# Kernel optimization log

Measured on AMD Instinct MI355X. Metric: run time of the kernel, lower is better.

## Reference

```python
import jax, jax.numpy as jnp
import numpy as np

B, T, P = 256, 1024, 32
HOME = 0  # home_idx from init_kwargs


def setup_inputs() -> dict:
    key = jax.random.key(0)
    k1, k2 = jax.random.split(key, 2)
    U = jax.random.normal(k1, (B, T, P), dtype=jnp.float32)
    A = jax.random.uniform(k2, (P, P), dtype=jnp.float32, minval=-0.01, maxval=0.01)
    bias = jnp.zeros((P,), dtype=jnp.float32)
    return {"unary_logits_btp": U, "A": A, "bias": bias}


def reference(unary_logits_btp, A, bias):
    """Constrained Viterbi decode (enforce at least one non-home state).
    State is (purpose p, visited-nonhome flag v in {0,1}). Returns paths (B,T) int32."""
    U = unary_logits_btp + bias  # (B,T,P), bias broadcast as in decode()
    Bn, Tn, Pn = U.shape
    NEG = jnp.finfo(U.dtype).min / 4
    is_home = jnp.arange(Pn) == HOME  # (P,)

    # t=0: v=0 only at home, v=1 only at non-home
    d0 = jnp.where(is_home, U[:, 0], NEG)
    d1 = jnp.where(is_home, NEG, U[:, 0])
    delta0 = jnp.stack([d0, d1], axis=-1)  # (B,P,2)

    def step(delta, U_t):
        # prev{v}[b, q, p] = delta[b, q, v] + A[q, p]
        prev0 = delta[:, :, 0][:, :, None] + A  # (B,P,P)
        prev1 = delta[:, :, 1][:, :, None] + A
        a0 = jnp.argmax(prev0, axis=1).astype(jnp.int32)
        v0 = jnp.max(prev0, axis=1)  # (B,P)
        a1 = jnp.argmax(prev1, axis=1).astype(jnp.int32)
        v1 = jnp.max(prev1, axis=1)
        use1 = v1 > v0  # strict >, matching torch.where(val_from1 > val_from0, ...)
        bval = jnp.where(use1, v1, v0)
        bq = jnp.where(use1, a1, a0)
        bv = use1.astype(jnp.int32)
        # next v=0 reachable only at home (from prev v=0)
        dn0 = jnp.where(is_home, v0 + U_t, NEG)
        # next v=1: home from prev v=1; non-home from best of prev v=0/v=1
        dn1 = jnp.where(is_home, v1, bval) + U_t
        p1 = jnp.where(is_home, a1, bq)
        vv1 = jnp.where(is_home, 1, bv).astype(jnp.int32)
        delta_new = jnp.stack([dn0, dn1], axis=-1)          # (B,P,2)
        psi_p = jnp.stack([a0, p1], axis=-1)                # (B,P,2) best prev purpose
        psi_v = jnp.stack([jnp.zeros_like(vv1), vv1], -1)   # (B,P,2) best prev flag
        return delta_new, (psi_p, psi_v)

    Us = jnp.swapaxes(U, 0, 1)  # (T,B,P)
    delta_T, (psi_p, psi_v) = jax.lax.scan(step, delta0, Us[1:])  # psi_*: (T-1,B,P,2)

    last_p = jnp.argmax(delta_T[:, :, 1], axis=1).astype(jnp.int32)  # (B,)
    b_idx = jnp.arange(Bn)

    def back(carry, psi):
        y, v = carry  # (B,), (B,)
        pp, pv = psi  # (B,P,2)
        py = pp[b_idx, y, v]
        nv = pv[b_idx, y, v]
        return (py, nv), py

    _, ys = jax.lax.scan(back, (last_p, jnp.ones((Bn,), jnp.int32)), (psi_p, psi_v),
                         reverse=True)  # ys: (T-1,B) with ys[t] = y[t]
    paths = jnp.concatenate([jnp.swapaxes(ys, 0, 1), last_p[:, None]], axis=1)  # (B,T)
    return paths
```

## Files before the change

### kernel.cpp

```cpp
#include <hip/hip_runtime.h>

#define T_LEN 1024
#define P_DIM 32
#define HOME_IDX 0
#define NCHUNK 32
#define CHUNK 32


__launch_bounds__(1024, 1)
__global__ void crf_viterbi_kernel(const float* __restrict__ U,
                                   const float* __restrict__ A,
                                   const float* __restrict__ bias,
                                   int* __restrict__ out)
{
    __shared__ __align__(16) float sdelta[P_DIM];
    __shared__ unsigned char spsi[(T_LEN - 1) * P_DIM];
    __shared__ unsigned char Mmap[NCHUNK * P_DIM];
    __shared__ unsigned char ent[NCHUNK];
    __shared__ int last_p_sh;

    const int tid = threadIdx.x;
    const int b   = blockIdx.x;
    int* __restrict__ outb = out + (size_t)b * T_LEN;

    if (tid < 64) {
        const int lane = tid;
        const int p    = lane & 31;
        const int h    = lane >> 5;
        const float NEG = -(3.4028234663852886e38f / 4.0f);

        float Areg[16];
#pragma unroll
        for (int j = 0; j < 16; ++j)
            Areg[j] = A[(16 * h + j) * P_DIM + p];
        const float A0p    = A[p];
        const float A00    = A[0];
        const float bias_p = bias[p];
        const float bias0  = bias[0];
        const int   q0     = h << 4;
        const bool  is_home = (p == HOME_IDX);

        const float4* __restrict__ sd4 = (const float4*)sdelta;

        const float* __restrict__ Ub = U + (size_t)b * T_LEN * P_DIM;

        const float u00 = Ub[p] + bias_p;
        float delta1  = is_home ? NEG : u00;
        float delta0h = Ub[HOME_IDX] + bias0;

        float L0 = Ub[1 * P_DIM + p];
        float L1 = Ub[2 * P_DIM + p];
        float L2 = Ub[3 * P_DIM + p];
        float L3 = Ub[4 * P_DIM + p];

        float Ut_n = L0 + bias_p;
        float u0_n = __shfl(Ut_n, 0);

        sdelta[p] = delta1;
        float4 R0 = sd4[4 * h + 0];
        float4 R1 = sd4[4 * h + 1];
        float4 R2 = sd4[4 * h + 2];
        float4 R3 = sd4[4 * h + 3];

#define STEP(t, Lc, Lr) do {                                                   \
    const float Ut  = Ut_n;                                                    \
    const float u0c = u0_n;                                                    \
    Ut_n = (Lc) + bias_p;                                                      \
    u0_n = __shfl(Ut_n, 0);                                                    \
    { int tn = (t) + 4; if (tn > T_LEN - 1) tn = T_LEN - 1;                    \
      (Lr) = Ub[(size_t)tn * P_DIM + p]; }                                     \
    float c[16];                                                               \
    c[0]  = R0.x + Areg[0];  c[1]  = R0.y + Areg[1];                           \
    c[2]  = R0.z + Areg[2];  c[3]  = R0.w + Areg[3];                           \
    c[4]  = R1.x + Areg[4];  c[5]  = R1.y + Areg[5];                           \
    c[6]  = R1.z + Areg[6];  c[7]  = R1.w + Areg[7];                           \
    c[8]  = R2.x + Areg[8];  c[9]  = R2.y + Areg[9];                           \
    c[10] = R2.z + Areg[10]; c[11] = R2.w + Areg[11];                          \
    c[12] = R3.x + Areg[12]; c[13] = R3.y + Areg[13];                          \
    c[14] = R3.z + Areg[14]; c[15] = R3.w + Areg[15];                          \
       \
    const float g0 = fmaxf(fmaxf(c[0],  c[1]),  c[2]);                         \
    const float g1 = fmaxf(fmaxf(c[3],  c[4]),  c[5]);                         \
    const float g2 = fmaxf(fmaxf(c[6],  c[7]),  c[8]);                         \
    const float g3 = fmaxf(fmaxf(c[9],  c[10]), c[11]);                        \
    const float g4 = fmaxf(fmaxf(c[12], c[13]), c[14]);                        \
    const float h0 = fmaxf(fmaxf(g0, g1), g2);                                 \
    const float h1 = fmaxf(fmaxf(g3, g4), c[15]);                              \
    const float bv = fmaxf(h0, h1);                                            \
                                                 \
    const float ovv = __shfl_xor(bv, 32);                                      \
    const float v1  = fmaxf(bv, ovv);                                          \
    const float v0  = delta0h + A0p;                                           \
    const bool  use1 = (v1 > v0);                    \
    const bool  cond = use1 || is_home;                                        \
    const float sel  = cond ? v1 : v0;                                         \
    const float dn1  = sel + Ut;                                               \
    delta0h = (delta0h + A00) + u0c;                                           \
       \
        \
    sdelta[p] = dn1;                                                           \
    R0 = sd4[4 * h + 0];                                                       \
    R1 = sd4[4 * h + 1];                                                       \
    R2 = sd4[4 * h + 2];                                                       \
    R3 = sd4[4 * h + 3];                                                       \
           \
    int ia = 99;                                                               \
    _Pragma("unroll")                                                          \
    for (int j = 15; j >= 0; --j)                                              \
        if (c[j] == v1) ia = q0 + j;                                           \
    const int oia = __shfl_xor(ia, 32);                                        \
    const int a1  = (ia < oia) ? ia : oia;                                     \
    const int bt  = cond ? (a1 | 32) : 0;                                      \
    spsi[(size_t)((t) - 1) * P_DIM + p] = (unsigned char)bt;                   \
    delta1 = dn1;                                                              \
} while (0)

        STEP(1, L1, L0);
        STEP(2, L2, L1);
        STEP(3, L3, L2);
        for (int t = 4; t <= T_LEN - 4; t += 4) {
            STEP(t + 0, L0, L3);
            STEP(t + 1, L1, L0);
            STEP(t + 2, L2, L1);
            STEP(t + 3, L3, L2);
        }
#undef STEP

        float mv = delta1;
        int   mi = p;
#pragma unroll
        for (int m = 16; m >= 1; m >>= 1) {
            float ov = __shfl_xor(mv, m);
            int   oi = __shfl_xor(mi, m);
            bool take = (ov > mv) || ((ov == mv) && (oi < mi));
            mv = take ? ov : mv;
            mi = take ? oi : mi;
        }
        if (lane == 0) {
            outb[T_LEN - 1] = mi;
            last_p_sh = mi;
        }
    }

    __syncthreads();

    {
        const int c  = tid >> 5;
        const int pp = tid & 31;
        const int i_hi = min((c + 1) * CHUNK, T_LEN - 1);
        const int i_lo = c * CHUNK;
        int y = pp, v = 1;
        for (int i = i_hi - 1; i >= i_lo; --i) {
            const int bt = spsi[i * P_DIM + y];
            const int py = v ? (bt & 31) : 0;
            const int nv = v ? ((bt >> 5) & 1) : 0;
            y = py; v = nv;
        }
        Mmap[c * P_DIM + pp] = (unsigned char)(y | (v << 5));
    }
    __syncthreads();

    if (tid == 0) {
        int y = last_p_sh, v = 1;
        for (int c = NCHUNK - 1; c >= 0; --c) {
            ent[c] = (unsigned char)(y | (v << 5));
            if (v) {
                const int m = Mmap[c * P_DIM + y];
                y = m & 31;
                v = (m >> 5) & 1;
            } else {
                y = 0; v = 0;
            }
        }
    }
    __syncthreads();

    if (tid < NCHUNK) {
        const int c = tid;
        const int i_hi = min((c + 1) * CHUNK, T_LEN - 1);
        const int i_lo = c * CHUNK;
        const int e = ent[c];
        int y = e & 31;
        int v = (e >> 5) & 1;
        for (int i = i_hi - 1; i >= i_lo; --i) {
            const int bt = spsi[i * P_DIM + y];
            const int py = v ? (bt & 31) : 0;
            const int nv = v ? ((bt >> 5) & 1) : 0;
            outb[i] = py;
            y = py; v = nv;
        }
    }
}

extern "C" void kernel_launch(void* const* d_in, const int* in_sizes, int n_in,
                              void* d_out, int out_size, void* d_ws, size_t ws_size,
                              hipStream_t stream) {
    const float* U    = (const float*)d_in[0];
    const float* A    = (const float*)d_in[1];
    const float* bias = (const float*)d_in[2];
    int* out = (int*)d_out;

    const int B = in_sizes[0] / (T_LEN * P_DIM);
    crf_viterbi_kernel<<<B, 1024, 0, stream>>>(U, A, bias, out);
}
```

Baseline: 309.2 us.

## Software-pipeline argmax backpointer computation across Viterbi steps

Defers the per-step argmax index search and backpointer store to the following steps, using double-buffered candidate arrays so the index search for step t overlaps the max chain of step t+1. The argmax now compares against each half's local max (not the combined max) and picks the winning half, which takes the index search off the critical serial dependency. It adds register pressure from two 16-float candidate arrays plus carried state, and epilogue code to drain the pipeline.

```diff
diff --git a/kernel.cpp b/kernel.cpp
--- a/kernel.cpp
+++ b/kernel.cpp
@@ -41,7 +41,6 @@
         const bool  is_home = (p == HOME_IDX);
 
         const float4* __restrict__ sd4 = (const float4*)sdelta;
-
         const float* __restrict__ Ub = U + (size_t)b * T_LEN * P_DIM;
 
         const float u00 = Ub[p] + bias_p;
@@ -62,69 +61,102 @@
         float4 R2 = sd4[4 * h + 2];
         float4 R3 = sd4[4 * h + 3];
 
-#define STEP(t, Lc, Lr) do {                                                   \
+        float cA[16], cB[16];
+        float bvp = 0.f, ovvp = 0.f, bv2 = 0.f, ovv2 = 0.f;
+        bool  condp = false, cond2 = false;
+        int   ia2 = 0, io2 = 0;
+
+#define STEP(t, F1, F2, CC, CP, Lc, Lr) do {                                   \
     const float Ut  = Ut_n;                                                    \
     const float u0c = u0_n;                                                    \
-    Ut_n = (Lc) + bias_p;                                                      \
-    u0_n = __shfl(Ut_n, 0);                                                    \
-    { int tn = (t) + 4; if (tn > T_LEN - 1) tn = T_LEN - 1;                    \
-      (Lr) = Ub[(size_t)tn * P_DIM + p]; }                                     \
-    float c[16];                                                               \
-    c[0]  = R0.x + Areg[0];  c[1]  = R0.y + Areg[1];                           \
-    c[2]  = R0.z + Areg[2];  c[3]  = R0.w + Areg[3];                           \
-    c[4]  = R1.x + Areg[4];  c[5]  = R1.y + Areg[5];                           \
-    c[6]  = R1.z + Areg[6];  c[7]  = R1.w + Areg[7];                           \
-    c[8]  = R2.x + Areg[8];  c[9]  = R2.y + Areg[9];                           \
-    c[10] = R2.z + Areg[10]; c[11] = R2.w + Areg[11];                          \
-    c[12] = R3.x + Areg[12]; c[13] = R3.y + Areg[13];                          \
-    c[14] = R3.z + Areg[14]; c[15] = R3.w + Areg[15];                          \
-       \
-    const float g0 = fmaxf(fmaxf(c[0],  c[1]),  c[2]);                         \
-    const float g1 = fmaxf(fmaxf(c[3],  c[4]),  c[5]);                         \
-    const float g2 = fmaxf(fmaxf(c[6],  c[7]),  c[8]);                         \
-    const float g3 = fmaxf(fmaxf(c[9],  c[10]), c[11]);                        \
-    const float g4 = fmaxf(fmaxf(c[12], c[13]), c[14]);                        \
+    CC[0]  = R0.x + Areg[0];  CC[1]  = R0.y + Areg[1];                         \
+    CC[2]  = R0.z + Areg[2];  CC[3]  = R0.w + Areg[3];                         \
+    CC[4]  = R1.x + Areg[4];  CC[5]  = R1.y + Areg[5];                         \
+    CC[6]  = R1.z + Areg[6];  CC[7]  = R1.w + Areg[7];                         \
+    CC[8]  = R2.x + Areg[8];  CC[9]  = R2.y + Areg[9];                         \
+    CC[10] = R2.z + Areg[10]; CC[11] = R2.w + Areg[11];                        \
+    CC[12] = R3.x + Areg[12]; CC[13] = R3.y + Areg[13];                        \
+    CC[14] = R3.z + Areg[14]; CC[15] = R3.w + Areg[15];                        \
+    const float g0 = fmaxf(fmaxf(CC[0],  CC[1]),  CC[2]);                      \
+    const float g1 = fmaxf(fmaxf(CC[3],  CC[4]),  CC[5]);                      \
+    const float g2 = fmaxf(fmaxf(CC[6],  CC[7]),  CC[8]);                      \
+    const float g3 = fmaxf(fmaxf(CC[9],  CC[10]), CC[11]);                     \
+    const float g4 = fmaxf(fmaxf(CC[12], CC[13]), CC[14]);                     \
     const float h0 = fmaxf(fmaxf(g0, g1), g2);                                 \
-    const float h1 = fmaxf(fmaxf(g3, g4), c[15]);                              \
+    const float h1 = fmaxf(fmaxf(g3, g4), CC[15]);                             \
     const float bv = fmaxf(h0, h1);                                            \
-                                                 \
+            \
     const float ovv = __shfl_xor(bv, 32);                                      \
-    const float v1  = fmaxf(bv, ovv);                                          \
-    const float v0  = delta0h + A0p;                                           \
+    int ia1 = 0, io1 = 0;                                                      \
+    if (F1) {        \
+        ia1 = q0 + 15;                                                         \
+        _Pragma("unroll")                                                      \
+        for (int j = 14; j >= 0; --j)                                          \
+            if (CP[j] == bvp) ia1 = q0 + j;                                    \
+        io1 = __shfl_xor(ia1, 32);                                             \
+    }                                                                          \
+    if (F2) {      \
+        const int amin = (ia2 < io2) ? ia2 : io2;                              \
+        int a1 = (bv2 > ovv2) ? ia2 : io2;                                     \
+        a1 = (bv2 == ovv2) ? amin : a1;                                        \
+        spsi[(size_t)((t) - 3) * P_DIM + p] =                                  \
+            (unsigned char)(cond2 ? (a1 | 32) : 0);                            \
+    }                                                                          \
+    const float v1 = fmaxf(bv, ovv);              \
+    const float v0 = delta0h + A0p;                                            \
     const bool  use1 = (v1 > v0);                    \
     const bool  cond = use1 || is_home;                                        \
     const float sel  = cond ? v1 : v0;                                         \
     const float dn1  = sel + Ut;                                               \
     delta0h = (delta0h + A00) + u0c;                                           \
-       \
         \
     sdelta[p] = dn1;                                                           \
     R0 = sd4[4 * h + 0];                                                       \
     R1 = sd4[4 * h + 1];                                                       \
     R2 = sd4[4 * h + 2];                                                       \
     R3 = sd4[4 * h + 3];                                                       \
-           \
-    int ia = 99;                                                               \
-    _Pragma("unroll")                                                          \
-    for (int j = 15; j >= 0; --j)                                              \
-        if (c[j] == v1) ia = q0 + j;                                           \
-    const int oia = __shfl_xor(ia, 32);                                        \
-    const int a1  = (ia < oia) ? ia : oia;                                     \
-    const int bt  = cond ? (a1 | 32) : 0;                                      \
-    spsi[(size_t)((t) - 1) * P_DIM + p] = (unsigned char)bt;                   \
+                                 \
+    Ut_n = (Lc) + bias_p;                                                      \
+    u0_n = __shfl(Ut_n, 0);                                                    \
+    { int tn = (t) + 4; if (tn > T_LEN - 1) tn = T_LEN - 1;                    \
+      (Lr) = Ub[(size_t)tn * P_DIM + p]; }                                     \
+                                                          \
+    bv2 = bvp; ovv2 = ovvp; cond2 = condp;                                     \
+    ia2 = ia1; io2 = io1;                                                      \
+    bvp = bv; ovvp = ovv; condp = cond;                                        \
     delta1 = dn1;                                                              \
 } while (0)
 
-        STEP(1, L1, L0);
-        STEP(2, L2, L1);
-        STEP(3, L3, L2);
+        STEP(1, 0, 0, cA, cB, L1, L0);
+        STEP(2, 1, 0, cB, cA, L2, L1);
+        STEP(3, 1, 1, cA, cB, L3, L2);
         for (int t = 4; t <= T_LEN - 4; t += 4) {
-            STEP(t + 0, L0, L3);
-            STEP(t + 1, L1, L0);
-            STEP(t + 2, L2, L1);
-            STEP(t + 3, L3, L2);
+            STEP(t + 0, 1, 1, cB, cA, L0, L3);
+            STEP(t + 1, 1, 1, cA, cB, L1, L0);
+            STEP(t + 2, 1, 1, cB, cA, L2, L1);
+            STEP(t + 3, 1, 1, cA, cB, L3, L2);
         }
 #undef STEP
+
+        {
+            const int amin = (ia2 < io2) ? ia2 : io2;
+            int a1 = (bv2 > ovv2) ? ia2 : io2;
+            a1 = (bv2 == ovv2) ? amin : a1;
+            spsi[(size_t)(T_LEN - 3) * P_DIM + p] =
+                (unsigned char)(cond2 ? (a1 | 32) : 0);
+        }
+        {
+            int ia = q0 + 15;
+#pragma unroll
+            for (int j = 14; j >= 0; --j)
+                if (cA[j] == bvp) ia = q0 + j;
+            const int oia  = __shfl_xor(ia, 32);
+            const int amin = (ia < oia) ? ia : oia;
+            int a1 = (bvp > ovvp) ? ia : oia;
+            a1 = (bvp == ovvp) ? amin : a1;
+            spsi[(size_t)(T_LEN - 2) * P_DIM + p] =
+                (unsigned char)(condp ? (a1 | 32) : 0);
+        }
 
         float mv = delta1;
         int   mi = p;
```

Result: no change. 304.5 us (-1.5%).
